# Kernel optimization log

Measured on AMD Instinct MI355X. Metric: run time of the kernel, lower is better.

The kernel has to match this reference:

```python
import jax, jax.numpy as jnp
import numpy as np
from jax import lax

SEQ, BATCH, FEAT = 64, 32768, 15
H1 = H2 = H3 = 4  # hidden sizes from the source module


def setup_inputs() -> dict:
    key = jax.random.key(0)
    ks = jax.random.split(key, 11)
    s = 0.1
    return {
        "x": jax.random.normal(ks[0], (SEQ, BATCH, FEAT), jnp.float32),
        "w1": jax.random.normal(ks[1], (H1, FEAT), jnp.float32) * s,
        "b1": jax.random.normal(ks[2], (H1,), jnp.float32) * s,
        "w2": jax.random.normal(ks[3], (H2, H1), jnp.float32) * s,
        "b2": jax.random.normal(ks[4], (H2,), jnp.float32) * s,
        "w_ih": jax.random.normal(ks[5], (4 * H3, H2), jnp.float32) * s,
        "w_hh": jax.random.normal(ks[6], (4 * H3, H3), jnp.float32) * s,
        "b_ih": jax.random.normal(ks[7], (4 * H3,), jnp.float32) * s,
        "b_hh": jax.random.normal(ks[8], (4 * H3,), jnp.float32) * s,
        "w3": jax.random.normal(ks[9], (1, H3), jnp.float32) * s,
        "b3": jax.random.normal(ks[10], (1,), jnp.float32) * s,
    }


def reference(x, w1, b1, w2, b2, w_ih, w_hh, b_ih, b_hh, w3, b3):
    seq, batch, _ = x.shape
    hidden = w_hh.shape[1]
    # front-end MLP: fc1 -> relu -> fc2 -> sigmoid   (applied per timestep)
    h1 = jax.nn.relu(jnp.einsum('sbf,hf->sbh', x, w1) + b1)          # [S,B,H1]
    h2 = jax.nn.sigmoid(jnp.einsum('sbh,gh->sbg', h1, w2) + b2)      # [S,B,H2]
    # precompute input-to-gate projections for all timesteps: [S,B,4H]
    gx = jnp.einsum('sbh,gh->sbg', h2, w_ih) + b_ih + b_hh

    def step(carry, gxt):
        h, c = carry
        gates = gxt + h @ w_hh.T                                      # [B,4H]
        i, f, g, o = jnp.split(gates, 4, axis=-1)                     # torch order i,f,g,o
        i = jax.nn.sigmoid(i)
        f = jax.nn.sigmoid(f)
        g = jnp.tanh(g)
        o = jax.nn.sigmoid(o)
        c = f * c + i * g
        h = o * jnp.tanh(c)
        return (h, c), None

    h0 = jnp.zeros((batch, hidden), x.dtype)
    c0 = jnp.zeros((batch, hidden), x.dtype)
    (h_last, _), _ = lax.scan(step, (h0, c0), gx)                     # last-step hidden [B,H3]
    out = jax.nn.sigmoid(h_last @ w3.T + b3)                          # [B,1]
    return out.reshape(batch)
```

## Files before the change

### kernel.cpp

```cpp
#include <hip/hip_runtime.h>

#define SEQ   64
#define BATCH 32768
#define FEAT  15
#define SLABBYTES (BATCH * FEAT * 4)

#define LOG2E 1.4426950408889634f

typedef float v2f __attribute__((ext_vector_type(2)));
typedef float v4f __attribute__((ext_vector_type(4)));

__device__ __forceinline__ float fast_rcp(float x) { return __builtin_amdgcn_rcpf(x); }
__device__ __forceinline__ float ex2(float x)      { return __builtin_amdgcn_exp2f(x); }
__device__ __forceinline__ float sig2(float t)     { return fast_rcp(1.0f + ex2(t)); }

template <int CTRL>
__device__ __forceinline__ float qmov(float v) {
    return __int_as_float(
        __builtin_amdgcn_mov_dpp(__float_as_int(v), CTRL, 0xf, 0xf, false));
}

__device__ __forceinline__ v2f fma2(v2f a, v2f b, v2f c) { return a * b + c; }

template <int N>
__device__ __forceinline__ void waitv() {
    asm volatile("s_waitcnt vmcnt(%0)" :: "n"(N) : "memory");
}

typedef const __attribute__((address_space(1))) void gas_t;
typedef __attribute__((address_space(3))) void las_t;

__global__ __launch_bounds__(256, 2) void lstm_fused(
    const float* __restrict__ x,
    const float* __restrict__ w1,  const float* __restrict__ b1,
    const float* __restrict__ w2,  const float* __restrict__ b2,
    const float* __restrict__ wih, const float* __restrict__ whh,
    const float* __restrict__ bih, const float* __restrict__ bhh,
    const float* __restrict__ w3,  const float* __restrict__ b3,
    float* __restrict__ out)
{
    __shared__ __align__(16) float lds[4][8][256];

    const int tid = threadIdx.x;
    const int w   = tid >> 6;
    const int l   = tid & 63;
    const int u   = l & 3;
    const int e   = l >> 2;
    const int ebase = blockIdx.x * 64 + w * 16;
    const int elem  = ebase + e;

    const int perm_e = (e + (e >> 2)) & 3;
    const int p      = (u - perm_e) & 3;
    const int inrow  = (p < 3) ? p * 16 : 44;
    uint32_t off = (uint32_t)(ebase + e) * 60u + (uint32_t)inrow;

    auto gload = [&](int b, uint32_t o) {
        __builtin_amdgcn_global_load_lds(
            (gas_t*)((const char*)x + o),
            (las_t*)&lds[w][b][0], 16, 0, 0);
    };

    int sb[4];
#pragma unroll
    for (int pp = 0; pp < 4; ++pp) sb[pp] = (4 * e + ((pp + perm_e) & 3)) * 4;

    auto ldrow = [&](int b, v4f& F0, v4f& F1, v4f& F2, v4f& F3) {
        const float* B = &lds[w][b][0];
        F0 = *(const v4f*)(B + sb[0]);
        F1 = *(const v4f*)(B + sb[1]);
        F2 = *(const v4f*)(B + sb[2]);
        F3 = *(const v4f*)(B + sb[3]);
    };

    v2f PA0, PA1, PA2, PA3, PB0, PB1, PB2, PB3, SEEDv;
    {
        const float* r = w1 + u * FEAT;
        PA0 = v2f{r[0],  r[1]};  PB0 = v2f{r[2],  r[3]};
        PA1 = v2f{r[4],  r[5]};  PB1 = v2f{r[6],  r[7]};
        PA2 = v2f{r[8],  r[9]};  PB2 = v2f{r[10], r[11]};
        PA3 = v2f{0.0f,  r[12]}; PB3 = v2f{r[13], r[14]};
        SEEDv = v2f{b1[u], 0.0f};
    }
    float W2s[4];
#pragma unroll
    for (int j = 0; j < 4; ++j) W2s[j] = -LOG2E * w2[u * 4 + j];
    const float B2v = -LOG2E * b2[u];
    v2f WIp[4][2], WHp[4][2], BIg[4];
#pragma unroll
    for (int g = 0; g < 4; ++g) {
        const float sg = (g == 2) ? (2.0f * LOG2E) : -LOG2E;
        const int row = (g * 4 + u) * 4;
        WIp[g][0] = v2f{sg * wih[row + 0], sg * wih[row + 1]};
        WIp[g][1] = v2f{sg * wih[row + 2], sg * wih[row + 3]};
        WHp[g][0] = v2f{sg * whh[row + 0], sg * whh[row + 1]};
        WHp[g][1] = v2f{sg * whh[row + 2], sg * whh[row + 3]};
        BIg[g]    = v2f{sg * (bih[g * 4 + u] + bhh[g * 4 + u]), 0.0f};
    }
    const float W3v = -LOG2E * w3[u];
    const float B3v = -LOG2E * b3[0];

    float h = 0.0f, c = 0.0f;

    auto step = [&](v4f F0, v4f F1, v4f F2, v4f F3) {
        v2f accA = fma2(PA0, F0.xy, fma2(PA1, F1.xy,
                   fma2(PA2, F2.xy, fma2(PA3, F3.xy, SEEDv))));
        v2f accB = fma2(PB0, F0.zw, fma2(PB1, F1.zw,
                   fma2(PB2, F2.zw, fma2(PB3, F3.zw, v2f{0.0f, 0.0f}))));
        const v2f accS = accA + accB;
        const float h1 = fmaxf(accS.x + accS.y, 0.0f);
        const float t0 = qmov<0x00>(h1), t1 = qmov<0x55>(h1);
        const float t2 = qmov<0xAA>(h1), t3 = qmov<0xFF>(h1);
        const float a2n = fmaf(W2s[0], t0, fmaf(W2s[1], t1,
                          fmaf(W2s[2], t2, fmaf(W2s[3], t3, B2v))));
        const float h2 = sig2(a2n);
        const v2f q01 = v2f{qmov<0x00>(h2), qmov<0x55>(h2)};
        const v2f q23 = v2f{qmov<0xAA>(h2), qmov<0xFF>(h2)};
        v2f A[4];
#pragma unroll
        for (int g = 0; g < 4; ++g)
            A[g] = fma2(WIp[g][0], q01, fma2(WIp[g][1], q23, BIg[g]));
        const v2f h01 = v2f{qmov<0x00>(h), qmov<0x55>(h)};
        const v2f h23 = v2f{qmov<0xAA>(h), qmov<0xFF>(h)};
#pragma unroll
        for (int g = 0; g < 4; ++g)
            A[g] = fma2(WHp[g][0], h01, fma2(WHp[g][1], h23, A[g]));
        const float ig = sig2(A[0].x + A[0].y);
        const float fg = sig2(A[1].x + A[1].y);
        const float gt = fmaf(-2.0f, sig2(A[2].x + A[2].y), 1.0f);
        const float og = sig2(A[3].x + A[3].y);
        c = fmaf(fg, c, ig * gt);
        const float tc = fmaf(-2.0f, sig2(c * (2.0f * LOG2E)), 1.0f);
        h = og * tc;
    };

#pragma unroll
    for (int b = 0; b < 6; ++b) { gload(b, off); off += SLABBYTES; }
    waitv<5>();
    __builtin_amdgcn_sched_barrier(0);
    v4f F0, F1, F2, F3;
    ldrow(0, F0, F1, F2, F3);

#pragma unroll 1
    for (int ph = 0; ph < 7; ++ph) {
#pragma unroll
        for (int j = 0; j < 8; ++j) {
            waitv<4>();
            __builtin_amdgcn_sched_barrier(0);
            v4f G0, G1, G2, G3;
            ldrow((j + 1) & 7, G0, G1, G2, G3);
            gload((j + 6) & 7, off);
            off += SLABBYTES;
            __builtin_amdgcn_sched_barrier(0);
            step(F0, F1, F2, F3);
            F0 = G0; F1 = G1; F2 = G2; F3 = G3;
        }
    }
#define EPI(JJ, NN)                                                   \
    {   waitv<NN>();                                                  \
        __builtin_amdgcn_sched_barrier(0);                            \
        v4f G0, G1, G2, G3;                                           \
        ldrow(((JJ) + 1) & 7, G0, G1, G2, G3);                        \
        step(F0, F1, F2, F3);                                         \
        F0 = G0; F1 = G1; F2 = G2; F3 = G3; }
    EPI(0, 4) EPI(1, 3) EPI(2, 2) EPI(3, 1) EPI(4, 0) EPI(5, 0) EPI(6, 0)
#undef EPI
    step(F0, F1, F2, F3);

    float pr = W3v * h;
    pr += qmov<0xB1>(pr);
    pr += qmov<0x4E>(pr);
    if (u == 0) out[elem] = sig2(pr + B3v);
}

extern "C" void kernel_launch(void* const* d_in, const int* in_sizes, int n_in,
                              void* d_out, int out_size, void* d_ws, size_t ws_size,
                              hipStream_t stream) {
    (void)in_sizes; (void)n_in; (void)d_ws; (void)ws_size; (void)out_size;
    const float* x   = (const float*)d_in[0];
    const float* w1  = (const float*)d_in[1];
    const float* b1  = (const float*)d_in[2];
    const float* w2  = (const float*)d_in[3];
    const float* b2  = (const float*)d_in[4];
    const float* wih = (const float*)d_in[5];
    const float* whh = (const float*)d_in[6];
    const float* bih = (const float*)d_in[7];
    const float* bhh = (const float*)d_in[8];
    const float* w3  = (const float*)d_in[9];
    const float* b3  = (const float*)d_in[10];
    float* out = (float*)d_out;

    lstm_fused<<<dim3(512), dim3(256), 0, stream>>>(
        x, w1, b1, w2, b2, wih, whh, bih, bhh, w3, b3, out);
}
```

Measured before the change: 29.75 us.

## Pipeline two timesteps per stage and use xor-permuted quad broadcasts

New measurement: 29.16 us, median of 2. -2.0%, faster.

```diff
diff --git a/kernel.cpp b/kernel.cpp
--- a/kernel.cpp
+++ b/kernel.cpp
@@ -81,25 +81,25 @@
         PA3 = v2f{0.0f,  r[12]}; PB3 = v2f{r[13], r[14]};
         SEEDv = v2f{b1[u], 0.0f};
     }
-    float W2s[4];
-#pragma unroll
-    for (int j = 0; j < 4; ++j) W2s[j] = -LOG2E * w2[u * 4 + j];
-    const float B2v = -LOG2E * b2[u];
-    v2f WIp[4][2], WHp[4][2], BIg[4];
+    const v2f W2X01 = v2f{-LOG2E * w2[u * 4 + u],       -LOG2E * w2[u * 4 + (u ^ 1)]};
+    const v2f W2X23 = v2f{-LOG2E * w2[u * 4 + (u ^ 2)], -LOG2E * w2[u * 4 + (u ^ 3)]};
+    const v2f B2seed = v2f{-LOG2E * b2[u], 0.0f};
+    v2f WIx[4][2], WHx[4][2], BIg[4];
 #pragma unroll
     for (int g = 0; g < 4; ++g) {
         const float sg = (g == 2) ? (2.0f * LOG2E) : -LOG2E;
         const int row = (g * 4 + u) * 4;
-        WIp[g][0] = v2f{sg * wih[row + 0], sg * wih[row + 1]};
-        WIp[g][1] = v2f{sg * wih[row + 2], sg * wih[row + 3]};
-        WHp[g][0] = v2f{sg * whh[row + 0], sg * whh[row + 1]};
-        WHp[g][1] = v2f{sg * whh[row + 2], sg * whh[row + 3]};
+        WIx[g][0] = v2f{sg * wih[row + u],       sg * wih[row + (u ^ 1)]};
+        WIx[g][1] = v2f{sg * wih[row + (u ^ 2)], sg * wih[row + (u ^ 3)]};
+        WHx[g][0] = v2f{sg * whh[row + u],       sg * whh[row + (u ^ 1)]};
+        WHx[g][1] = v2f{sg * whh[row + (u ^ 2)], sg * whh[row + (u ^ 3)]};
         BIg[g]    = v2f{sg * (bih[g * 4 + u] + bhh[g * 4 + u]), 0.0f};
     }
     const float W3v = -LOG2E * w3[u];
     const float B3v = -LOG2E * b3[0];
 
-    float h = 0.0f, c = 0.0f;
+    float h = 0.0f;
+    float cs = 0.0f;
 
     auto step = [&](v4f F0, v4f F1, v4f F2, v4f F3) {
         v2f accA = fma2(PA0, F0.xy, fma2(PA1, F1.xy,
@@ -108,63 +108,89 @@
                    fma2(PB2, F2.zw, fma2(PB3, F3.zw, v2f{0.0f, 0.0f}))));
         const v2f accS = accA + accB;
         const float h1 = fmaxf(accS.x + accS.y, 0.0f);
-        const float t0 = qmov<0x00>(h1), t1 = qmov<0x55>(h1);
-        const float t2 = qmov<0xAA>(h1), t3 = qmov<0xFF>(h1);
-        const float a2n = fmaf(W2s[0], t0, fmaf(W2s[1], t1,
-                          fmaf(W2s[2], t2, fmaf(W2s[3], t3, B2v))));
-        const float h2 = sig2(a2n);
-        const v2f q01 = v2f{qmov<0x00>(h2), qmov<0x55>(h2)};
-        const v2f q23 = v2f{qmov<0xAA>(h2), qmov<0xFF>(h2)};
+        const v2f H01 = v2f{h1, qmov<0xB1>(h1)};
+        const v2f H23 = v2f{qmov<0x4E>(h1), qmov<0x1B>(h1)};
+        const v2f a2 = fma2(W2X01, H01, fma2(W2X23, H23, B2seed));
+        const float h2 = sig2(a2.x + a2.y);
+        const v2f Q01 = v2f{h2, qmov<0xB1>(h2)};
+        const v2f Q23 = v2f{qmov<0x4E>(h2), qmov<0x1B>(h2)};
+        const v2f P01 = v2f{h, qmov<0xB1>(h)};
+        const v2f P23 = v2f{qmov<0x4E>(h), qmov<0x1B>(h)};
         v2f A[4];
 #pragma unroll
         for (int g = 0; g < 4; ++g)
-            A[g] = fma2(WIp[g][0], q01, fma2(WIp[g][1], q23, BIg[g]));
-        const v2f h01 = v2f{qmov<0x00>(h), qmov<0x55>(h)};
-        const v2f h23 = v2f{qmov<0xAA>(h), qmov<0xFF>(h)};
-#pragma unroll
-        for (int g = 0; g < 4; ++g)
-            A[g] = fma2(WHp[g][0], h01, fma2(WHp[g][1], h23, A[g]));
+            A[g] = fma2(WIx[g][0], Q01, fma2(WIx[g][1], Q23,
+                   fma2(WHx[g][0], P01, fma2(WHx[g][1], P23, BIg[g]))));
         const float ig = sig2(A[0].x + A[0].y);
         const float fg = sig2(A[1].x + A[1].y);
-        const float gt = fmaf(-2.0f, sig2(A[2].x + A[2].y), 1.0f);
+        const float gt2 = fmaf(-4.0f * LOG2E, sig2(A[2].x + A[2].y), 2.0f * LOG2E);
         const float og = sig2(A[3].x + A[3].y);
-        c = fmaf(fg, c, ig * gt);
-        const float tc = fmaf(-2.0f, sig2(c * (2.0f * LOG2E)), 1.0f);
+        cs = fmaf(fg, cs, ig * gt2);
+        const float tc = fmaf(-2.0f, sig2(cs), 1.0f);
         h = og * tc;
     };
 
 #pragma unroll
     for (int b = 0; b < 6; ++b) { gload(b, off); off += SLABBYTES; }
-    waitv<5>();
-    __builtin_amdgcn_sched_barrier(0);
-    v4f F0, F1, F2, F3;
+    waitv<4>();
+    v4f F0, F1, F2, F3, G0, G1, G2, G3;
     ldrow(0, F0, F1, F2, F3);
+    ldrow(1, G0, G1, G2, G3);
 
 #pragma unroll 1
     for (int ph = 0; ph < 7; ++ph) {
 #pragma unroll
-        for (int j = 0; j < 8; ++j) {
-            waitv<4>();
-            __builtin_amdgcn_sched_barrier(0);
-            v4f G0, G1, G2, G3;
-            ldrow((j + 1) & 7, G0, G1, G2, G3);
-            gload((j + 6) & 7, off);
-            off += SLABBYTES;
+        for (int d = 0; d < 4; ++d) {
+            waitv<2>();
+            v4f N0, N1, N2, N3, M0, M1, M2, M3;
+            ldrow((2 * d + 2) & 7, N0, N1, N2, N3);
+            ldrow((2 * d + 3) & 7, M0, M1, M2, M3);
+            gload((2 * d + 6) & 7, off);  off += SLABBYTES;
+            gload((2 * d + 7) & 7, off);  off += SLABBYTES;
             __builtin_amdgcn_sched_barrier(0);
             step(F0, F1, F2, F3);
-            F0 = G0; F1 = G1; F2 = G2; F3 = G3;
+            step(G0, G1, G2, G3);
+            F0 = N0; F1 = N1; F2 = N2; F3 = N3;
+            G0 = M0; G1 = M1; G2 = M2; G3 = M3;
         }
     }
-#define EPI(JJ, NN)                                                   \
-    {   waitv<NN>();                                                  \
-        __builtin_amdgcn_sched_barrier(0);                            \
-        v4f G0, G1, G2, G3;                                           \
-        ldrow(((JJ) + 1) & 7, G0, G1, G2, G3);                        \
-        step(F0, F1, F2, F3);                                         \
-        F0 = G0; F1 = G1; F2 = G2; F3 = G3; }
-    EPI(0, 4) EPI(1, 3) EPI(2, 2) EPI(3, 1) EPI(4, 0) EPI(5, 0) EPI(6, 0)
-#undef EPI
+    {
+        waitv<2>();
+        v4f N0, N1, N2, N3, M0, M1, M2, M3;
+        ldrow(2, N0, N1, N2, N3);
+        ldrow(3, M0, M1, M2, M3);
+        gload(6, off);  off += SLABBYTES;
+        gload(7, off);  off += SLABBYTES;
+        __builtin_amdgcn_sched_barrier(0);
+        step(F0, F1, F2, F3);
+        step(G0, G1, G2, G3);
+        F0 = N0; F1 = N1; F2 = N2; F3 = N3;
+        G0 = M0; G1 = M1; G2 = M2; G3 = M3;
+    }
+    {
+        waitv<2>();
+        v4f N0, N1, N2, N3, M0, M1, M2, M3;
+        ldrow(4, N0, N1, N2, N3);
+        ldrow(5, M0, M1, M2, M3);
+        __builtin_amdgcn_sched_barrier(0);
+        step(F0, F1, F2, F3);
+        step(G0, G1, G2, G3);
+        F0 = N0; F1 = N1; F2 = N2; F3 = N3;
+        G0 = M0; G1 = M1; G2 = M2; G3 = M3;
+    }
+    {
+        waitv<0>();
+        v4f N0, N1, N2, N3, M0, M1, M2, M3;
+        ldrow(6, N0, N1, N2, N3);
+        ldrow(7, M0, M1, M2, M3);
+        __builtin_amdgcn_sched_barrier(0);
+        step(F0, F1, F2, F3);
+        step(G0, G1, G2, G3);
+        F0 = N0; F1 = N1; F2 = N2; F3 = N3;
+        G0 = M0; G1 = M1; G2 = M2; G3 = M3;
+    }
     step(F0, F1, F2, F3);
+    step(G0, G1, G2, G3);
 
     float pr = W3v * h;
     pr += qmov<0xB1>(pr);
```

## Process two batch elements per thread with packed math and butterfly DPP broadcasts

Applied to the files above, without the earlier changes.

New measurement: 29.81 us. About the same (+0.2%).

```diff
diff --git a/kernel.cpp b/kernel.cpp
--- a/kernel.cpp
+++ b/kernel.cpp
@@ -19,8 +19,14 @@
     return __int_as_float(
         __builtin_amdgcn_mov_dpp(__float_as_int(v), CTRL, 0xf, 0xf, false));
 }
+template <int CTRL>
+__device__ __forceinline__ v2f qmov2(v2f v) {
+    return v2f{qmov<CTRL>(v.x), qmov<CTRL>(v.y)};
+}
 
 __device__ __forceinline__ v2f fma2(v2f a, v2f b, v2f c) { return a * b + c; }
+__device__ __forceinline__ v2f sig2p(v2f t) { return v2f{sig2(t.x), sig2(t.y)}; }
+__device__ __forceinline__ v2f sp(float v)  { return v2f{v, v}; }
 
 template <int N>
 __device__ __forceinline__ void waitv() {
@@ -30,7 +36,7 @@
 typedef const __attribute__((address_space(1))) void gas_t;
 typedef __attribute__((address_space(3))) void las_t;
 
-__global__ __launch_bounds__(256, 2) void lstm_fused(
+__global__ __launch_bounds__(256, 1) void lstm_fused(
     const float* __restrict__ x,
     const float* __restrict__ w1,  const float* __restrict__ b1,
     const float* __restrict__ w2,  const float* __restrict__ b2,
@@ -39,38 +45,35 @@
     const float* __restrict__ w3,  const float* __restrict__ b3,
     float* __restrict__ out)
 {
-    __shared__ __align__(16) float lds[4][8][256];
+    __shared__ __align__(16) float lds[4][8][512];
 
     const int tid = threadIdx.x;
     const int w   = tid >> 6;
     const int l   = tid & 63;
     const int u   = l & 3;
-    const int e   = l >> 2;
-    const int ebase = blockIdx.x * 64 + w * 16;
-    const int elem  = ebase + e;
-
-    const int perm_e = (e + (e >> 2)) & 3;
-    const int p      = (u - perm_e) & 3;
+    const int q   = l >> 2;
+    const int ebase = (blockIdx.x * 4 + w) * 32;
+    const int elemA = ebase + q;
+    const int elemB = ebase + 16 + q;
+
+    const int perm_q = (q + (q >> 2)) & 3;
+    const int p      = (u - perm_q) & 3;
     const int inrow  = (p < 3) ? p * 16 : 44;
-    uint32_t off = (uint32_t)(ebase + e) * 60u + (uint32_t)inrow;
-
-    auto gload = [&](int b, uint32_t o) {
+    uint32_t off = (uint32_t)(ebase + q) * 60u + (uint32_t)inrow;
+
+    auto gload2 = [&](int b) {
         __builtin_amdgcn_global_load_lds(
-            (gas_t*)((const char*)x + o),
-            (las_t*)&lds[w][b][0], 16, 0, 0);
+            (gas_t*)((const char*)x + off),
+            (las_t*)&lds[w][b][0],   16, 0, 0);
+        __builtin_amdgcn_global_load_lds(
+            (gas_t*)((const char*)x + off + 960u),
+            (las_t*)&lds[w][b][256], 16, 0, 0);
+        off += SLABBYTES;
     };
 
     int sb[4];
 #pragma unroll
-    for (int pp = 0; pp < 4; ++pp) sb[pp] = (4 * e + ((pp + perm_e) & 3)) * 4;
-
-    auto ldrow = [&](int b, v4f& F0, v4f& F1, v4f& F2, v4f& F3) {
-        const float* B = &lds[w][b][0];
-        F0 = *(const v4f*)(B + sb[0]);
-        F1 = *(const v4f*)(B + sb[1]);
-        F2 = *(const v4f*)(B + sb[2]);
-        F3 = *(const v4f*)(B + sb[3]);
-    };
+    for (int pp = 0; pp < 4; ++pp) sb[pp] = (4 * q + ((pp + perm_q) & 3)) * 4;
 
     v2f PA0, PA1, PA2, PA3, PB0, PB1, PB2, PB3, SEEDv;
     {
@@ -81,95 +84,118 @@
         PA3 = v2f{0.0f,  r[12]}; PB3 = v2f{r[13], r[14]};
         SEEDv = v2f{b1[u], 0.0f};
     }
-    float W2s[4];
-#pragma unroll
-    for (int j = 0; j < 4; ++j) W2s[j] = -LOG2E * w2[u * 4 + j];
-    const float B2v = -LOG2E * b2[u];
-    v2f WIp[4][2], WHp[4][2], BIg[4];
+    v2f W2q[4], B2q;
+#pragma unroll
+    for (int k = 0; k < 4; ++k) W2q[k] = sp(-LOG2E * w2[u * 4 + (u ^ k)]);
+    B2q = sp(-LOG2E * b2[u]);
+    v2f WIq[4][4], WHq[4][4], BIq[4];
 #pragma unroll
     for (int g = 0; g < 4; ++g) {
         const float sg = (g == 2) ? (2.0f * LOG2E) : -LOG2E;
         const int row = (g * 4 + u) * 4;
-        WIp[g][0] = v2f{sg * wih[row + 0], sg * wih[row + 1]};
-        WIp[g][1] = v2f{sg * wih[row + 2], sg * wih[row + 3]};
-        WHp[g][0] = v2f{sg * whh[row + 0], sg * whh[row + 1]};
-        WHp[g][1] = v2f{sg * whh[row + 2], sg * whh[row + 3]};
-        BIg[g]    = v2f{sg * (bih[g * 4 + u] + bhh[g * 4 + u]), 0.0f};
+#pragma unroll
+        for (int k = 0; k < 4; ++k) {
+            WIq[g][k] = sp(sg * wih[row + (u ^ k)]);
+            WHq[g][k] = sp(sg * whh[row + (u ^ k)]);
+        }
+        BIq[g] = sp(sg * (bih[g * 4 + u] + bhh[g * 4 + u]));
     }
     const float W3v = -LOG2E * w3[u];
     const float B3v = -LOG2E * b3[0];
 
-    float h = 0.0f, c = 0.0f;
-
-    auto step = [&](v4f F0, v4f F1, v4f F2, v4f F3) {
-        v2f accA = fma2(PA0, F0.xy, fma2(PA1, F1.xy,
-                   fma2(PA2, F2.xy, fma2(PA3, F3.xy, SEEDv))));
-        v2f accB = fma2(PB0, F0.zw, fma2(PB1, F1.zw,
-                   fma2(PB2, F2.zw, fma2(PB3, F3.zw, v2f{0.0f, 0.0f}))));
-        const v2f accS = accA + accB;
-        const float h1 = fmaxf(accS.x + accS.y, 0.0f);
-        const float t0 = qmov<0x00>(h1), t1 = qmov<0x55>(h1);
-        const float t2 = qmov<0xAA>(h1), t3 = qmov<0xFF>(h1);
-        const float a2n = fmaf(W2s[0], t0, fmaf(W2s[1], t1,
-                          fmaf(W2s[2], t2, fmaf(W2s[3], t3, B2v))));
-        const float h2 = sig2(a2n);
-        const v2f q01 = v2f{qmov<0x00>(h2), qmov<0x55>(h2)};
-        const v2f q23 = v2f{qmov<0xAA>(h2), qmov<0xFF>(h2)};
+    v2f hp  = v2f{0.0f, 0.0f};
+    v2f csp = v2f{0.0f, 0.0f};
+
+    auto step = [&](v4f FA0, v4f FA1, v4f FA2, v4f FA3,
+                    v4f FB0, v4f FB1, v4f FB2, v4f FB3) {
+        v2f aA = fma2(PA0, FA0.xy, fma2(PA1, FA1.xy,
+                 fma2(PA2, FA2.xy, fma2(PA3, FA3.xy, SEEDv))));
+        v2f bA = fma2(PB0, FA0.zw, fma2(PB1, FA1.zw,
+                 fma2(PB2, FA2.zw, fma2(PB3, FA3.zw, v2f{0.0f, 0.0f}))));
+        v2f aB = fma2(PA0, FB0.xy, fma2(PA1, FB1.xy,
+                 fma2(PA2, FB2.xy, fma2(PA3, FB3.xy, SEEDv))));
+        v2f bB = fma2(PB0, FB0.zw, fma2(PB1, FB1.zw,
+                 fma2(PB2, FB2.zw, fma2(PB3, FB3.zw, v2f{0.0f, 0.0f}))));
+        const v2f sA = aA + bA, sB = aB + bB;
+        const v2f h1p = v2f{fmaxf(sA.x + sA.y, 0.0f), fmaxf(sB.x + sB.y, 0.0f)};
+        const v2f H1 = qmov2<0xB1>(h1p), H2 = qmov2<0x4E>(h1p), H3 = qmov2<0x1B>(h1p);
+        const v2f a2p = fma2(W2q[0], h1p, fma2(W2q[1], H1,
+                        fma2(W2q[2], H2, fma2(W2q[3], H3, B2q))));
+        const v2f h2p = sig2p(a2p);
+        const v2f Q1 = qmov2<0xB1>(h2p), Q2 = qmov2<0x4E>(h2p), Q3 = qmov2<0x1B>(h2p);
+        const v2f P1 = qmov2<0xB1>(hp),  P2 = qmov2<0x4E>(hp),  P3 = qmov2<0x1B>(hp);
         v2f A[4];
 #pragma unroll
         for (int g = 0; g < 4; ++g)
-            A[g] = fma2(WIp[g][0], q01, fma2(WIp[g][1], q23, BIg[g]));
-        const v2f h01 = v2f{qmov<0x00>(h), qmov<0x55>(h)};
-        const v2f h23 = v2f{qmov<0xAA>(h), qmov<0xFF>(h)};
-#pragma unroll
-        for (int g = 0; g < 4; ++g)
-            A[g] = fma2(WHp[g][0], h01, fma2(WHp[g][1], h23, A[g]));
-        const float ig = sig2(A[0].x + A[0].y);
-        const float fg = sig2(A[1].x + A[1].y);
-        const float gt = fmaf(-2.0f, sig2(A[2].x + A[2].y), 1.0f);
-        const float og = sig2(A[3].x + A[3].y);
-        c = fmaf(fg, c, ig * gt);
-        const float tc = fmaf(-2.0f, sig2(c * (2.0f * LOG2E)), 1.0f);
-        h = og * tc;
+            A[g] = fma2(WIq[g][0], h2p, fma2(WIq[g][1], Q1,
+                   fma2(WIq[g][2], Q2,  fma2(WIq[g][3], Q3,
+                   fma2(WHq[g][0], hp,  fma2(WHq[g][1], P1,
+                   fma2(WHq[g][2], P2,  fma2(WHq[g][3], P3, BIq[g]))))))));
+        const v2f igp  = sig2p(A[0]);
+        const v2f fgp  = sig2p(A[1]);
+        const v2f gt2p = fma2(sp(-4.0f * LOG2E), sig2p(A[2]), sp(2.0f * LOG2E));
+        const v2f ogp  = sig2p(A[3]);
+        csp = fma2(fgp, csp, igp * gt2p);
+        const v2f tcp = fma2(sp(-2.0f), sig2p(csp), sp(1.0f));
+        hp = ogp * tcp;
     };
 
-#pragma unroll
-    for (int b = 0; b < 6; ++b) { gload(b, off); off += SLABBYTES; }
-    waitv<5>();
-    __builtin_amdgcn_sched_barrier(0);
-    v4f F0, F1, F2, F3;
-    ldrow(0, F0, F1, F2, F3);
+#define LDROW(b, A0, A1, A2, A3, B0, B1, B2, B3)                     \
+    {   const float* Bp = &lds[w][(b)][0];                           \
+        A0 = *(const v4f*)(Bp + sb[0]);                              \
+        A1 = *(const v4f*)(Bp + sb[1]);                              \
+        A2 = *(const v4f*)(Bp + sb[2]);                              \
+        A3 = *(const v4f*)(Bp + sb[3]);                              \
+        B0 = *(const v4f*)(Bp + 256 + sb[0]);                        \
+        B1 = *(const v4f*)(Bp + 256 + sb[1]);                        \
+        B2 = *(const v4f*)(Bp + 256 + sb[2]);                        \
+        B3 = *(const v4f*)(Bp + 256 + sb[3]);  }
+
+#pragma unroll
+    for (int b = 0; b < 6; ++b) gload2(b);
+    waitv<10>();
+    v4f FA0, FA1, FA2, FA3, FB0, FB1, FB2, FB3;
+    LDROW(0, FA0, FA1, FA2, FA3, FB0, FB1, FB2, FB3);
 
 #pragma unroll 1
     for (int ph = 0; ph < 7; ++ph) {
 #pragma unroll
         for (int j = 0; j < 8; ++j) {
-            waitv<4>();
-            __builtin_amdgcn_sched_barrier(0);
-            v4f G0, G1, G2, G3;
-            ldrow((j + 1) & 7, G0, G1, G2, G3);
-            gload((j + 6) & 7, off);
-            off += SLABBYTES;
-            __builtin_amdgcn_sched_barrier(0);
-            step(F0, F1, F2, F3);
-            F0 = G0; F1 = G1; F2 = G2; F3 = G3;
+            waitv<8>();
+            v4f NA0, NA1, NA2, NA3, NB0, NB1, NB2, NB3;
+            LDROW((j + 1) & 7, NA0, NA1, NA2, NA3, NB0, NB1, NB2, NB3);
+            gload2((j + 6) & 7);
+            step(FA0, FA1, FA2, FA3, FB0, FB1, FB2, FB3);
+            FA0 = NA0; FA1 = NA1; FA2 = NA2; FA3 = NA3;
+            FB0 = NB0; FB1 = NB1; FB2 = NB2; FB3 = NB3;
         }
     }
-#define EPI(JJ, NN)                                                   \
+#define TAIL(BN, GB, NN)                                              \
     {   waitv<NN>();                                                  \
-        __builtin_amdgcn_sched_barrier(0);                            \
-        v4f G0, G1, G2, G3;                                           \
-        ldrow(((JJ) + 1) & 7, G0, G1, G2, G3);                        \
-        step(F0, F1, F2, F3);                                         \
-        F0 = G0; F1 = G1; F2 = G2; F3 = G3; }
-    EPI(0, 4) EPI(1, 3) EPI(2, 2) EPI(3, 1) EPI(4, 0) EPI(5, 0) EPI(6, 0)
-#undef EPI
-    step(F0, F1, F2, F3);
-
-    float pr = W3v * h;
-    pr += qmov<0xB1>(pr);
-    pr += qmov<0x4E>(pr);
-    if (u == 0) out[elem] = sig2(pr + B3v);
+        v4f NA0, NA1, NA2, NA3, NB0, NB1, NB2, NB3;                   \
+        LDROW((BN), NA0, NA1, NA2, NA3, NB0, NB1, NB2, NB3);          \
+        if ((GB) >= 0) gload2(GB);                                    \
+        step(FA0, FA1, FA2, FA3, FB0, FB1, FB2, FB3);                 \
+        FA0 = NA0; FA1 = NA1; FA2 = NA2; FA3 = NA3;                   \
+        FB0 = NB0; FB1 = NB1; FB2 = NB2; FB3 = NB3;  }
+    TAIL(1, 6, 8)
+    TAIL(2, 7, 8)
+    TAIL(3, -1, 8)
+    TAIL(4, -1, 6)
+    TAIL(5, -1, 4)
+    TAIL(6, -1, 2)
+    TAIL(7, -1, 0)
+#undef TAIL
+    step(FA0, FA1, FA2, FA3, FB0, FB1, FB2, FB3);
+#undef LDROW
+
+    v2f prp = sp(W3v) * hp;
+    prp += qmov2<0xB1>(prp);
+    prp += qmov2<0x4E>(prp);
+    if (u == 0) {
+        out[elemA] = sig2(prp.x + B3v);
+        out[elemB] = sig2(prp.y + B3v);
+    }
 }
 
 extern "C" void kernel_launch(void* const* d_in, const int* in_sizes, int n_in,
@@ -189,6 +215,6 @@
     const float* b3  = (const float*)d_in[10];
     float* out = (float*)d_out;
 
-    lstm_fused<<<dim3(512), dim3(256), 0, stream>>>(
+    lstm_fused<<<dim3(256), dim3(256), 0, stream>>>(
         x, w1, b1, w2, b2, wih, whh, bih, bhh, w3, b3, out);
 }
```
